# Performance work log

Hardware: AMD Instinct MI355X
Metric: run time of the kernel (lower is better)

## Reference

```python
import jax, jax.numpy as jnp
import numpy as np


def conv1x1(x, W, b):
    # 1x1 Conv2d == per-pixel linear over channels. x: [B,C,H,W], W: [O,C], b: [O]
    return jnp.einsum('oc,bchw->bohw', W, x) + b[None, :, None, None]


def setup_inputs() -> dict:
    key = jax.random.key(0)
    ks = jax.random.split(key, 18)
    B, C, Hd, H, W = 16, 64, 64, 32, 32
    s = 0.05
    f = jax.random.normal
    return {
        'h': f(ks[0], (B, C, H, W), jnp.float32),
        'm': f(ks[1], (B, C, H, W), jnp.float32),
        'Wq': f(ks[2], (Hd, C), jnp.float32) * s,
        'bq': f(ks[3], (Hd,), jnp.float32) * s,
        'Wk': f(ks[4], (Hd, C), jnp.float32) * s,
        'bk': f(ks[5], (Hd,), jnp.float32) * s,
        'Wk2': f(ks[6], (Hd, C), jnp.float32) * s,
        'bk2': f(ks[7], (Hd,), jnp.float32) * s,
        'Wv': f(ks[8], (C, C), jnp.float32) * s,
        'bv': f(ks[9], (C,), jnp.float32) * s,
        'Wv2': f(ks[10], (C, C), jnp.float32) * s,
        'bv2': f(ks[11], (C,), jnp.float32) * s,
        'Wz': f(ks[12], (2 * C, 2 * C), jnp.float32) * s,
        'bz': f(ks[13], (2 * C,), jnp.float32) * s,
        'Wm': f(ks[14], (3 * C, 3 * C), jnp.float32) * s,
        'bm': f(ks[15], (3 * C,), jnp.float32) * s,
    }


def reference(h, m, Wq, bq, Wk, bk, Wk2, bk2, Wv, bv, Wv2, bv2, Wz, bz, Wm, bm):
    B, C, H, W = h.shape
    Hd = Wq.shape[0]
    N = H * W
    # Shared query from h
    Q_h = conv1x1(h, Wq, bq).reshape(B, Hd, N).transpose(0, 2, 1)  # [B,N,Hd]
    # Self-attention branch over h
    K_h = conv1x1(h, Wk, bk).reshape(B, Hd, N)                     # [B,Hd,N]
    A_h = jax.nn.softmax(jnp.einsum('bnd,bdm->bnm', Q_h, K_h), axis=-1)  # [B,N,N]
    V_h = conv1x1(h, Wv, bv).reshape(B, C, N)                      # [B,C,N]
    Z_h = jnp.einsum('bnm,bcm->bcn', A_h, V_h).reshape(B, C, H, W)
    # Cross-attention branch over memory m (same query Q_h)
    K_m = conv1x1(m, Wk2, bk2).reshape(B, Hd, N)
    A_m = jax.nn.softmax(jnp.einsum('bnd,bdm->bnm', Q_h, K_m), axis=-1)
    V_m = conv1x1(m, Wv2, bv2).reshape(B, C, N)
    Z_m = jnp.einsum('bnm,bcm->bcn', A_m, V_m).reshape(B, C, H, W)
    # Fuse and gated memory update
    Z = conv1x1(jnp.concatenate([Z_h, Z_m], axis=1), Wz, bz)       # [B,2C,H,W]
    combined = conv1x1(jnp.concatenate([Z, h], axis=1), Wm, bm)    # [B,3C,H,W]
    mo, mg, mi = combined[:, :C], combined[:, C:2 * C], combined[:, 2 * C:]
    mi = jax.nn.sigmoid(mi)
    new_m = (1 - mi) * m + mi * jnp.tanh(mg)
    new_h = jax.nn.sigmoid(mo) * new_m
    return (new_h, new_m)
```

## Files before the change

### kernel.cpp

```cpp
#include <hip/hip_runtime.h>

typedef unsigned short u16;
typedef unsigned int u32;
typedef __attribute__((ext_vector_type(8))) short bf16x8;
typedef __attribute__((ext_vector_type(4))) short bf16x4;
typedef __attribute__((ext_vector_type(4))) float f32x4;

#define MFMA(a, b, c) __builtin_amdgcn_mfma_f32_16x16x32_bf16((a), (b), (c), 0, 0, 0)
#define MFMA16(a, b, c) __builtin_amdgcn_mfma_f32_16x16x16bf16_1k((a), (b), (c), 0, 0, 0)

static __device__ __forceinline__ u16 f2bf(float x) {
  u32 u = __float_as_uint(x);
  u += 0x7FFFu + ((u >> 16) & 1u);
  return (u16)(u >> 16);
}
static __device__ __forceinline__ u32 packbf_t(float hi, float lo) {
  return __builtin_amdgcn_perm(__float_as_uint(hi), __float_as_uint(lo), 0x07060302u);
}
static __device__ __forceinline__ u32 packbf(float lo, float hi) {
  return (u32)f2bf(lo) | ((u32)f2bf(hi) << 16);
}

__global__ __launch_bounds__(256) void proj_kernel(
    const float* __restrict__ h, const float* __restrict__ m_,
    const float* __restrict__ bq, const float* __restrict__ bk,
    const float* __restrict__ bk2, const float* __restrict__ bv,
    const float* __restrict__ bv2,
    const float* __restrict__ Wq, const float* __restrict__ Wk,
    const float* __restrict__ Wk2, const float* __restrict__ Wv,
    const float* __restrict__ Wv2,
    const float* __restrict__ Wz, const float* __restrict__ Wm,
    const float* __restrict__ bm,
    u16* __restrict__ Qb, u16* __restrict__ Khb, u16* __restrict__ Kmb,
    u16* __restrict__ Vhb, u16* __restrict__ Vmb, u16* __restrict__ hbuf,
    u16* __restrict__ Wzb, u16* __restrict__ Wmb, float* __restrict__ bmp)
{
  const int tid = threadIdx.x;
  const int b = blockIdx.y, n0 = blockIdx.x * 64, z = blockIdx.z;

  {
    const int gid = (blockIdx.z * 256 + blockIdx.y * 16 + blockIdx.x) * 256 + tid;
    if (gid < 16384) {
      Wzb[gid] = f2bf(Wz[gid]);
    } else if (gid < 53248) {
      const int e = gid - 16384;
      const int p = e / 192, k = e % 192;
      const int hb2 = p / 96, r1 = p % 96, ctl = r1 / 48, r2 = r1 % 48;
      const int g = r2 >> 4, mm = r2 & 15;
      const int o = g * 64 + (hb2 * 2 + ctl) * 16 + mm;
      Wmb[p * 192 + k] = f2bf(Wm[o * 192 + k]);
    } else if (gid < 53440) {
      const int p = gid - 53248;
      const int hb2 = p / 96, r1 = p % 96, ctl = r1 / 48, r2 = r1 % 48;
      const int g = r2 >> 4, mm = r2 & 15;
      const int o = g * 64 + (hb2 * 2 + ctl) * 16 + mm;
      bmp[p] = bm[o];
    }
  }

  __shared__ __align__(16) u16 xt[64][72];
  const float* __restrict__ X = (z >= 3) ? m_ : h;

  {
    const int px = tid & 63, c0 = (tid >> 6) * 16;
#pragma unroll
    for (int i = 0; i < 8; ++i) {
      const int c = c0 + 2 * i;
      const float f0 = X[(b * 64 + c) * 1024 + n0 + px];
      const float f1 = X[(b * 64 + c + 1) * 1024 + n0 + px];
      *(u32*)&xt[px][c] = packbf(f0, f1);
    }
  }
  __syncthreads();

  const int lane = tid & 63, w = tid >> 6;
  const int mm = lane & 15, q = lane >> 4;

  const bf16x8 xa0 = *(const bf16x8*)&xt[w * 16 + mm][q * 8];
  const bf16x8 xa1 = *(const bf16x8*)&xt[w * 16 + mm][32 + q * 8];

  auto ldw8 = [&](const float* Wf, int row, int col0) {
    const float4 a = *(const float4*)(Wf + row * 64 + col0);
    const float4 bb = *(const float4*)(Wf + row * 64 + col0 + 4);
    union { u32 u[4]; bf16x8 v; } r;
    r.u[0] = packbf(a.x, a.y);
    r.u[1] = packbf(a.z, a.w);
    r.u[2] = packbf(bb.x, bb.y);
    r.u[3] = packbf(bb.z, bb.w);
    return r.v;
  };

  auto qk_store = [&](u16* dst, const float* Wf, const float* bias) {
#pragma unroll
    for (int ot = 0; ot < 4; ++ot) {
      const bf16x8 wb0 = ldw8(Wf, ot * 16 + mm, q * 8);
      const bf16x8 wb1 = ldw8(Wf, ot * 16 + mm, 32 + q * 8);
      const float4 b4 = *(const float4*)(bias + ot * 16 + q * 4);
      f32x4 d = {b4.x, b4.y, b4.z, b4.w};
      d = MFMA(wb0, xa0, d);
      d = MFMA(wb1, xa1, d);
      uint2 val;
      val.x = packbf(d[0], d[1]);
      val.y = packbf(d[2], d[3]);
      *(uint2*)(dst + (b * 1024 + n0 + w * 16 + mm) * 64 + ot * 16 + q * 4) = val;
    }
  };
  auto v_store = [&](u16* dst, const float* Wf, const float* bias) {
#pragma unroll
    for (int ot = 0; ot < 4; ++ot) {
      const bf16x8 wb0 = ldw8(Wf, ot * 16 + mm, q * 8);
      const bf16x8 wb1 = ldw8(Wf, ot * 16 + mm, 32 + q * 8);
      const float bb = bias[ot * 16 + mm];
      f32x4 d = {bb, bb, bb, bb};
      d = MFMA(xa0, wb0, d);
      d = MFMA(xa1, wb1, d);
      uint2 val;
      val.x = packbf(d[0], d[1]);
      val.y = packbf(d[2], d[3]);
      *(uint2*)(dst + b * 65536 + blockIdx.x * 4096 + (ot * 16 + mm) * 64 +
                w * 16 + q * 4) = val;
    }
  };

  if (z == 0) {
    qk_store(Qb, Wq, bq);
    const int px = tid >> 2, sg = tid & 3;
    u32* dst = (u32*)(hbuf + (b * 1024 + n0 + px) * 64 + sg * 16);
    const u16* srcr = &xt[px][sg * 16];
#pragma unroll
    for (int j = 0; j < 8; ++j) dst[j] = *(const u32*)(srcr + 2 * j);
  } else if (z == 1) {
    qk_store(Khb, Wk, bk);
  } else if (z == 2) {
    v_store(Vhb, Wv, bv);
  } else if (z == 3) {
    qk_store(Kmb, Wk2, bk2);
  } else {
    v_store(Vmb, Wv2, bv2);
  }
}

__global__ __launch_bounds__(256, 4) void attn_kernel(
    const u16* __restrict__ Qb, const u16* __restrict__ Khb,
    const u16* __restrict__ Kmb, const u16* __restrict__ Vhb,
    const u16* __restrict__ Vmb, u16* __restrict__ Ztb)
{
  const int id = blockIdx.x;
  const int b = id & 15;
  const int br = (id >> 4) & 1;
  const int qh = id >> 5;
  const u16* __restrict__ K = (br ? Kmb : Khb) + b * 65536;
  const u16* __restrict__ V = (br ? Vmb : Vhb) + b * 65536;

  __shared__ __align__(16) u16 pool[18432];
  __shared__ float rsw[4][32];
  u16* const Kl = pool;
  u16* const Vl = pool + 9216;

  const int tid = threadIdx.x, w = tid >> 6, lane = tid & 63;
  const int mm = lane & 15, q = lane >> 4;
  const int q0 = qh * 32;

  bf16x8 qb0[2], qb1[2];
#pragma unroll
  for (int qt = 0; qt < 2; ++qt) {
    const u16* Qp = Qb + (b * 1024 + q0 + qt * 16 + mm) * 64;
    qb0[qt] = *(const bf16x8*)(Qp + q * 8);
    qb1[qt] = *(const bf16x8*)(Qp + 32 + q * 8);
  }

  f32x4 z[2][4];
#pragma unroll
  for (int qt = 0; qt < 2; ++qt)
#pragma unroll
    for (int ct = 0; ct < 4; ++ct) z[qt][ct] = (f32x4){0.f, 0.f, 0.f, 0.f};
  float rp[2] = {0.f, 0.f};

  const int so0 = (tid >> 3) * 72 + (tid & 7) * 8;
  const int so1 = so0 + 32 * 72;
  uint4 sk0, sk1, sv0, sv1;
  auto stage_load = [&](int kc) {
    const u16* Ks = K + kc * 4096;
    const u16* Vs = V + kc * 4096;
    sk0 = *(const uint4*)(Ks + tid * 8);
    sk1 = *(const uint4*)(Ks + tid * 8 + 2048);
    sv0 = *(const uint4*)(Vs + tid * 8);
    sv1 = *(const uint4*)(Vs + tid * 8 + 2048);
  };
  auto stage_store = [&](int buf) {
    u16* Kd = Kl + buf * 4608;
    u16* Vd = Vl + buf * 4608;
    *(uint4*)(Kd + so0) = sk0;
    *(uint4*)(Kd + so1) = sk1;
    *(uint4*)(Vd + so0) = sv0;
    *(uint4*)(Vd + so1) = sv1;
  };

  stage_load(0);
  stage_store(0);
  __syncthreads();

  int cur = 0;
#pragma unroll 1
  for (int kc = 0; kc < 16; ++kc) {
    if (kc < 15) stage_load(kc + 1);

    const u16* Kc = Kl + cur * 4608;
    const u16* Vc = Vl + cur * 4608;
    const bf16x8 kf0 = *(const bf16x8*)(Kc + (w * 16 + mm) * 72 + q * 8);
    const bf16x8 kf1 = *(const bf16x8*)(Kc + (w * 16 + mm) * 72 + 32 + q * 8);
    bf16x4 vf[4];
#pragma unroll
    for (int ct = 0; ct < 4; ++ct)
      vf[ct] = *(const bf16x4*)(Vc + (ct * 16 + mm) * 72 + w * 16 + q * 4);

#pragma unroll
    for (int qt = 0; qt < 2; ++qt) {
      f32x4 s = {0.f, 0.f, 0.f, 0.f};
      s = MFMA(kf0, qb0[qt], s);
      s = MFMA(kf1, qb1[qt], s);
      const float e0 = __expf(s[0]), e1 = __expf(s[1]);
      const float e2 = __expf(s[2]), e3 = __expf(s[3]);
      rp[qt] += (e0 + e1) + (e2 + e3);
      union { u32 u[2]; bf16x4 v; } pb;
      pb.u[0] = packbf_t(e1, e0);
      pb.u[1] = packbf_t(e3, e2);
#pragma unroll
      for (int ct = 0; ct < 4; ++ct) z[qt][ct] = MFMA16(vf[ct], pb.v, z[qt][ct]);
    }

    if (kc < 15) stage_store(cur ^ 1);
    __syncthreads();
    cur ^= 1;
  }

  u16* const zcb = pool;
#pragma unroll
  for (int qt = 0; qt < 2; ++qt) {
    float v = rp[qt];
    v += __shfl_xor(v, 16);
    v += __shfl_xor(v, 32);
    if (q == 0) rsw[w][qt * 16 + mm] = v;
#pragma unroll
    for (int ct = 0; ct < 4; ++ct) {
      uint2 val;
      val.x = packbf_t(z[qt][ct][1], z[qt][ct][0]);
      val.y = packbf_t(z[qt][ct][3], z[qt][ct][2]);
      *(uint2*)(zcb + w * 2176 + (qt * 16 + mm) * 68 + ct * 16 + q * 4) = val;
    }
  }
  __syncthreads();

  const int c2 = tid & 31, qr = tid >> 5;
#pragma unroll
  for (int i = 0; i < 4; ++i) {
    const int query = qr + i * 8;
    const float rt = rsw[0][query] + rsw[1][query] + rsw[2][query] + rsw[3][query];
    const float rinv = __builtin_amdgcn_rcpf(rt);
    float vlo = 0.f, vhi = 0.f;
#pragma unroll
    for (int ww = 0; ww < 4; ++ww) {
      const u32 u = *(const u32*)(zcb + ww * 2176 + query * 68 + c2 * 2);
      vlo += __uint_as_float(u << 16);
      vhi += __uint_as_float(u & 0xffff0000u);
    }
    vlo *= rinv;
    vhi *= rinv;
    *(u32*)(Ztb + (b * 1024 + q0 + query) * 128 + br * 64 + c2 * 2) = packbf_t(vhi, vlo);
  }
}

__global__ __launch_bounds__(256) void tail_kernel(
    const u16* __restrict__ Ztb, const u16* __restrict__ hbuf,
    const float* __restrict__ m_, const u16* __restrict__ Wzb,
    const float* __restrict__ bz, const u16* __restrict__ Wmb,
    const float* __restrict__ bmp, float* __restrict__ out)
{
  const int b = blockIdx.y, n0 = blockIdx.x * 16;
  __shared__ __align__(16) u16 zp[16][136];
  const int tid = threadIdx.x, lane = tid & 63, wv = tid >> 6;
  const int mm = lane & 15, q = lane >> 4;

  {
    bf16x8 za[4];
#pragma unroll
    for (int ks = 0; ks < 4; ++ks)
      za[ks] = *(const bf16x8*)(Ztb + (b * 1024 + n0 + mm) * 128 + ks * 32 + q * 8);
#pragma unroll
    for (int ot = 0; ot < 2; ++ot) {
      const int o0 = wv * 32 + ot * 16;
      const float4 b4 = *(const float4*)(bz + o0 + q * 4);
      f32x4 d = {b4.x, b4.y, b4.z, b4.w};
#pragma unroll
      for (int ks = 0; ks < 4; ++ks) {
        const bf16x8 wb = *(const bf16x8*)(Wzb + (o0 + mm) * 128 + ks * 32 + q * 8);
        d = MFMA(wb, za[ks], d);
      }
      uint2 val;
      val.x = packbf(d[0], d[1]);
      val.y = packbf(d[2], d[3]);
      *(uint2*)&zp[mm][o0 + q * 4] = val;
    }
  }
  __syncthreads();

  {
    bf16x8 fa[6];
#pragma unroll
    for (int ks = 0; ks < 4; ++ks)
      fa[ks] = *(const bf16x8*)&zp[mm][ks * 32 + q * 8];
    {
      const u16* hp = hbuf + (b * 1024 + n0 + mm) * 64;
      fa[4] = *(const bf16x8*)(hp + q * 8);
      fa[5] = *(const bf16x8*)(hp + 32 + q * 8);
    }
    f32x4 dd[3];
#pragma unroll
    for (int j = 0; j < 3; ++j) {
      const int p = wv * 48 + j * 16 + mm;
      const float bb = bmp[p];
      f32x4 d = {bb, bb, bb, bb};
#pragma unroll
      for (int ks = 0; ks < 6; ++ks) {
        const bf16x8 wb = *(const bf16x8*)(Wmb + p * 192 + ks * 32 + q * 8);
        d = MFMA(fa[ks], wb, d);
      }
      dd[j] = d;
    }
    const int c = wv * 16 + mm;
    const int px = n0 + q * 4;
    const float4 mold = *(const float4*)(m_ + (b * 64 + c) * 1024 + px);
    float4 nh, nm;
#pragma unroll
    for (int r = 0; r < 4; ++r) {
      const float xo = dd[0][r];
      const float xg = dd[1][r];
      const float xi = dd[2][r];
      const float si = __builtin_amdgcn_rcpf(1.f + __expf(-xi));
      const float th = 1.f - 2.f * __builtin_amdgcn_rcpf(__expf(2.f * xg) + 1.f);
      const float so = __builtin_amdgcn_rcpf(1.f + __expf(-xo));
      const float mo = ((const float*)&mold)[r];
      const float nmv = (1.f - si) * mo + si * th;
      ((float*)&nm)[r] = nmv;
      ((float*)&nh)[r] = so * nmv;
    }
    *(float4*)(out + (b * 64 + c) * 1024 + px) = nh;
    *(float4*)(out + 1048576 + (b * 64 + c) * 1024 + px) = nm;
  }
}

extern "C" void kernel_launch(void* const* d_in, const int* in_sizes, int n_in,
                              void* d_out, int out_size, void* d_ws, size_t ws_size,
                              hipStream_t stream) {
  const float* h   = (const float*)d_in[0];
  const float* m   = (const float*)d_in[1];
  const float* Wq  = (const float*)d_in[2];
  const float* bq  = (const float*)d_in[3];
  const float* Wk  = (const float*)d_in[4];
  const float* bk  = (const float*)d_in[5];
  const float* Wk2 = (const float*)d_in[6];
  const float* bk2 = (const float*)d_in[7];
  const float* Wv  = (const float*)d_in[8];
  const float* bv  = (const float*)d_in[9];
  const float* Wv2 = (const float*)d_in[10];
  const float* bv2 = (const float*)d_in[11];
  const float* Wz  = (const float*)d_in[12];
  const float* bz  = (const float*)d_in[13];
  const float* Wm  = (const float*)d_in[14];
  const float* bm  = (const float*)d_in[15];
  float* out = (float*)d_out;

  char* ws = (char*)d_ws;
  const size_t MB = 1024 * 1024;
  u16* Qb   = (u16*)(ws + 0 * MB);
  u16* Khb  = (u16*)(ws + 2 * MB);
  u16* Kmb  = (u16*)(ws + 4 * MB);
  u16* Vhb  = (u16*)(ws + 6 * MB);
  u16* Vmb  = (u16*)(ws + 8 * MB);
  u16* hbuf = (u16*)(ws + 10 * MB);
  u16* Ztb  = (u16*)(ws + 12 * MB);
  u16* Wzb  = (u16*)(ws + 16 * MB + 40960);
  u16* Wmb  = (u16*)(ws + 16 * MB + 73728);
  float* bmp = (float*)(ws + 16 * MB + 147456);

  proj_kernel<<<dim3(16, 16, 5), 256, 0, stream>>>(
      h, m, bq, bk, bk2, bv, bv2, Wq, Wk, Wk2, Wv, Wv2, Wz, Wm, bm,
      Qb, Khb, Kmb, Vhb, Vmb, hbuf, Wzb, Wmb, bmp);
  attn_kernel<<<1024, 256, 0, stream>>>(Qb, Khb, Kmb, Vhb, Vmb, Ztb);
  tail_kernel<<<dim3(64, 16), 256, 0, stream>>>(Ztb, hbuf, m, Wzb, bz, Wmb, bmp, out);
}
```

Before: 138.5 us.

## Double queries per attention block and prefetch two K/V chunks ahead

Each attention block now handles 64 queries instead of 32, halving the grid to 512 blocks so every K/V chunk staged in shared memory is reused across twice as many queries. The staging loop is unrolled by two, with two register sets so global loads run further ahead of compute. The launch-bounds occupancy hint is dropped to allow the extra accumulator registers. The cost is higher register pressure, lower occupancy and fewer blocks to spread across the CUs.

```diff
diff --git a/kernel.cpp b/kernel.cpp
--- a/kernel.cpp
+++ b/kernel.cpp
@@ -140,7 +140,7 @@
   }
 }
 
-__global__ __launch_bounds__(256, 4) void attn_kernel(
+__global__ __launch_bounds__(256) void attn_kernel(
     const u16* __restrict__ Qb, const u16* __restrict__ Khb,
     const u16* __restrict__ Kmb, const u16* __restrict__ Vhb,
     const u16* __restrict__ Vmb, u16* __restrict__ Ztb)
@@ -153,58 +153,53 @@
   const u16* __restrict__ V = (br ? Vmb : Vhb) + b * 65536;
 
   __shared__ __align__(16) u16 pool[18432];
-  __shared__ float rsw[4][32];
+  __shared__ float rsw[4][64];
   u16* const Kl = pool;
   u16* const Vl = pool + 9216;
 
   const int tid = threadIdx.x, w = tid >> 6, lane = tid & 63;
   const int mm = lane & 15, q = lane >> 4;
-  const int q0 = qh * 32;
-
-  bf16x8 qb0[2], qb1[2];
-#pragma unroll
-  for (int qt = 0; qt < 2; ++qt) {
+  const int q0 = qh * 64;
+
+  bf16x8 qb0[4], qb1[4];
+#pragma unroll
+  for (int qt = 0; qt < 4; ++qt) {
     const u16* Qp = Qb + (b * 1024 + q0 + qt * 16 + mm) * 64;
     qb0[qt] = *(const bf16x8*)(Qp + q * 8);
     qb1[qt] = *(const bf16x8*)(Qp + 32 + q * 8);
   }
 
-  f32x4 z[2][4];
-#pragma unroll
-  for (int qt = 0; qt < 2; ++qt)
+  f32x4 z[4][4];
+#pragma unroll
+  for (int qt = 0; qt < 4; ++qt)
 #pragma unroll
     for (int ct = 0; ct < 4; ++ct) z[qt][ct] = (f32x4){0.f, 0.f, 0.f, 0.f};
-  float rp[2] = {0.f, 0.f};
+  float rp[4] = {0.f, 0.f, 0.f, 0.f};
 
   const int so0 = (tid >> 3) * 72 + (tid & 7) * 8;
   const int so1 = so0 + 32 * 72;
-  uint4 sk0, sk1, sv0, sv1;
-  auto stage_load = [&](int kc) {
+
+  uint4 ka0, ka1, va0, va1;
+  uint4 kb0, kb1, vb0, vb1;
+  auto ld = [&](int kc, uint4& r0, uint4& r1, uint4& s0, uint4& s1) {
     const u16* Ks = K + kc * 4096;
     const u16* Vs = V + kc * 4096;
-    sk0 = *(const uint4*)(Ks + tid * 8);
-    sk1 = *(const uint4*)(Ks + tid * 8 + 2048);
-    sv0 = *(const uint4*)(Vs + tid * 8);
-    sv1 = *(const uint4*)(Vs + tid * 8 + 2048);
-  };
-  auto stage_store = [&](int buf) {
+    r0 = *(const uint4*)(Ks + tid * 8);
+    r1 = *(const uint4*)(Ks + tid * 8 + 2048);
+    s0 = *(const uint4*)(Vs + tid * 8);
+    s1 = *(const uint4*)(Vs + tid * 8 + 2048);
+  };
+  auto st = [&](int buf, const uint4& r0, const uint4& r1, const uint4& s0,
+                const uint4& s1) {
     u16* Kd = Kl + buf * 4608;
     u16* Vd = Vl + buf * 4608;
-    *(uint4*)(Kd + so0) = sk0;
-    *(uint4*)(Kd + so1) = sk1;
-    *(uint4*)(Vd + so0) = sv0;
-    *(uint4*)(Vd + so1) = sv1;
-  };
-
-  stage_load(0);
-  stage_store(0);
-  __syncthreads();
-
-  int cur = 0;
-#pragma unroll 1
-  for (int kc = 0; kc < 16; ++kc) {
-    if (kc < 15) stage_load(kc + 1);
-
+    *(uint4*)(Kd + so0) = r0;
+    *(uint4*)(Kd + so1) = r1;
+    *(uint4*)(Vd + so0) = s0;
+    *(uint4*)(Vd + so1) = s1;
+  };
+
+  auto compute = [&](int cur) {
     const u16* Kc = Kl + cur * 4608;
     const u16* Vc = Vl + cur * 4608;
     const bf16x8 kf0 = *(const bf16x8*)(Kc + (w * 16 + mm) * 72 + q * 8);
@@ -215,7 +210,7 @@
       vf[ct] = *(const bf16x4*)(Vc + (ct * 16 + mm) * 72 + w * 16 + q * 4);
 
 #pragma unroll
-    for (int qt = 0; qt < 2; ++qt) {
+    for (int qt = 0; qt < 4; ++qt) {
       f32x4 s = {0.f, 0.f, 0.f, 0.f};
       s = MFMA(kf0, qb0[qt], s);
       s = MFMA(kf1, qb1[qt], s);
@@ -228,15 +223,28 @@
 #pragma unroll
       for (int ct = 0; ct < 4; ++ct) z[qt][ct] = MFMA16(vf[ct], pb.v, z[qt][ct]);
     }
-
-    if (kc < 15) stage_store(cur ^ 1);
+  };
+
+  ld(0, ka0, ka1, va0, va1);
+  st(0, ka0, ka1, va0, va1);
+  ld(1, ka0, ka1, va0, va1);
+  __syncthreads();
+
+#pragma unroll 1
+  for (int kc = 0; kc < 16; kc += 2) {
+    if (kc + 2 < 16) ld(kc + 2, kb0, kb1, vb0, vb1);
+    compute(0);
+    st(1, ka0, ka1, va0, va1);
     __syncthreads();
-    cur ^= 1;
+    if (kc + 3 < 16) ld(kc + 3, ka0, ka1, va0, va1);
+    compute(1);
+    if (kc + 2 < 16) st(0, kb0, kb1, vb0, vb1);
+    __syncthreads();
   }
 
   u16* const zcb = pool;
 #pragma unroll
-  for (int qt = 0; qt < 2; ++qt) {
+  for (int qt = 0; qt < 4; ++qt) {
     float v = rp[qt];
     v += __shfl_xor(v, 16);
     v += __shfl_xor(v, 32);
@@ -246,21 +254,21 @@
       uint2 val;
       val.x = packbf_t(z[qt][ct][1], z[qt][ct][0]);
       val.y = packbf_t(z[qt][ct][3], z[qt][ct][2]);
-      *(uint2*)(zcb + w * 2176 + (qt * 16 + mm) * 68 + ct * 16 + q * 4) = val;
+      *(uint2*)(zcb + w * 4352 + (qt * 16 + mm) * 68 + ct * 16 + q * 4) = val;
     }
   }
   __syncthreads();
 
   const int c2 = tid & 31, qr = tid >> 5;
 #pragma unroll
-  for (int i = 0; i < 4; ++i) {
+  for (int i = 0; i < 8; ++i) {
     const int query = qr + i * 8;
     const float rt = rsw[0][query] + rsw[1][query] + rsw[2][query] + rsw[3][query];
     const float rinv = __builtin_amdgcn_rcpf(rt);
     float vlo = 0.f, vhi = 0.f;
 #pragma unroll
     for (int ww = 0; ww < 4; ++ww) {
-      const u32 u = *(const u32*)(zcb + ww * 2176 + query * 68 + c2 * 2);
+      const u32 u = *(const u32*)(zcb + ww * 4352 + query * 68 + c2 * 2);
       vlo += __uint_as_float(u << 16);
       vhi += __uint_as_float(u & 0xffff0000u);
     }
@@ -386,6 +394,6 @@
   proj_kernel<<<dim3(16, 16, 5), 256, 0, stream>>>(
       h, m, bq, bk, bk2, bv, bv2, Wq, Wk, Wk2, Wv, Wv2, Wz, Wm, bm,
       Qb, Khb, Kmb, Vhb, Vmb, hbuf, Wzb, Wmb, bmp);
-  attn_kernel<<<1024, 256, 0, stream>>>(Qb, Khb, Kmb, Vhb, Vmb, Ztb);
+  attn_kernel<<<512, 256, 0, stream>>>(Qb, Khb, Kmb, Vhb, Vmb, Ztb);
   tail_kernel<<<dim3(64, 16), 256, 0, stream>>>(Ztb, hbuf, m, Wzb, bz, Wmb, bmp, out);
 }
```

After: 140.4 us. About the same (+1.4%).
